# Kernel optimization log

Measured on AMD Instinct MI355X. Metric: run time of the kernel, lower is better.

The kernel has to match this reference:

```python
import jax, jax.numpy as jnp
import numpy as np

N_SRC0, N_FTRS, N_HID, N_CLS = 200000, 128, 1500, 64
E0, E1 = 1600000, 500000
RES0, RES1 = 50000, 10000


def sage_conv(x, src, tgt, res_size, W_root, W_neigh, b):
    # mean aggregation of neighbor (source) features onto the first res_size target nodes
    msg = x[src]                                              # [E, F] gather
    summed = jax.ops.segment_sum(msg, tgt, num_segments=res_size)   # [res, F]
    cnt = jax.ops.segment_sum(jnp.ones((src.shape[0],), x.dtype), tgt, num_segments=res_size)
    mean = summed / jnp.maximum(cnt, 1.0)[:, None]
    return x[:res_size] @ W_root + mean @ W_neigh + b


def setup_inputs() -> dict:
    key = jax.random.key(0)
    ks = jax.random.split(key, 12)
    x = jax.random.normal(ks[0], (N_SRC0, N_FTRS), dtype=jnp.float32)
    edge_src0 = jax.random.randint(ks[1], (E0,), 0, N_SRC0)
    edge_tgt0 = jax.random.randint(ks[2], (E0,), 0, RES0)
    edge_src1 = jax.random.randint(ks[3], (E1,), 0, RES0)
    edge_tgt1 = jax.random.randint(ks[4], (E1,), 0, RES1)
    s1 = 1.0 / np.sqrt(N_FTRS)
    s2 = 1.0 / np.sqrt(N_HID)
    W1_root = jax.random.uniform(ks[5], (N_FTRS, N_HID), jnp.float32, -s1, s1)
    W1_neigh = jax.random.uniform(ks[6], (N_FTRS, N_HID), jnp.float32, -s1, s1)
    b1 = jax.random.uniform(ks[7], (N_HID,), jnp.float32, -s1, s1)
    W2_root = jax.random.uniform(ks[8], (N_HID, N_CLS), jnp.float32, -s2, s2)
    W2_neigh = jax.random.uniform(ks[9], (N_HID, N_CLS), jnp.float32, -s2, s2)
    b2 = jax.random.uniform(ks[10], (N_CLS,), jnp.float32, -s2, s2)
    return {
        "x": x,
        "W1_root": W1_root, "W1_neigh": W1_neigh, "b1": b1,
        "W2_root": W2_root, "W2_neigh": W2_neigh, "b2": b2,
        "edge_src0": edge_src0, "edge_tgt0": edge_tgt0,
        "edge_src1": edge_src1, "edge_tgt1": edge_tgt1,
        "res0": RES0, "res1": RES1,
    }


def reference(x, W1_root, W1_neigh, b1, W2_root, W2_neigh, b2,
              edge_src0, edge_tgt0, edge_src1, edge_tgt1, res0, res1):
    h = sage_conv(x, edge_src0, edge_tgt0, res0, W1_root, W1_neigh, b1)  # [res0, H]
    h = jax.nn.relu(h)
    # dropout p=0.5 is identity in eval mode
    out = sage_conv(h, edge_src1, edge_tgt1, res1, W2_root, W2_neigh, b2)  # [res1, C]
    return jax.nn.log_softmax(out, axis=1)
```

## Files before the change

kernel.cpp:

```cpp
#include <hip/hip_runtime.h>
#include <hip/hip_bf16.h>
#include <cstdint>
#include <cstddef>

#define NSRC   200000
#define NF     128
#define NHID   1500
#define NHIDP  1536
#define NCLS   64
#define E0N    1600000
#define E1N    500000
#define RES0   50000
#define RES1   10000

#define CH     4096
#define NCH0   ((E0N + CH - 1) / CH)
#define NCH1   ((E1N + CH - 1) / CH)
#define NB0    ((RES0 + 255) / 256)
#define NB1    ((RES1 + 255) / 256)

#define PREP_BLOCKS  ((256 * NHIDP + 128 * NHIDP + NHIDP + 255) / 256)
#define COPYX_BLOCKS ((NSRC * NF) / (256 * 8))

typedef __bf16 bf16x8 __attribute__((ext_vector_type(8)));
typedef float  f32x4  __attribute__((ext_vector_type(4)));
typedef unsigned short u16x8 __attribute__((ext_vector_type(8)));
typedef unsigned int u32;
typedef unsigned long long u64;

__device__ __forceinline__ unsigned short f2bf(float f) {
    union { float f; unsigned u; } v; v.f = f;
    unsigned r = v.u + 0x7fffu + ((v.u >> 16) & 1u);
    return (unsigned short)(r >> 16);
}
__device__ __forceinline__ float bf2f(unsigned short b) {
    union { u32 u; float f; } v; v.u = ((u32)b) << 16;
    return v.f;
}

__device__ __forceinline__ void lds_dma16(const void* g, void* lds) {
    __builtin_amdgcn_global_load_lds(
        (const __attribute__((address_space(1))) unsigned int*)g,
        (__attribute__((address_space(3))) unsigned int*)lds, 16, 0, 0);
}

__device__ __forceinline__ void raw_barrier() {
    __asm__ volatile("s_barrier" ::: "memory");
}
__device__ __forceinline__ void wait_vm4() {
    __asm__ volatile("s_waitcnt vmcnt(4)" ::: "memory");
}
__device__ __forceinline__ void wait_vm0() {
    __asm__ volatile("s_waitcnt vmcnt(0)" ::: "memory");
}
__device__ __forceinline__ void wait_lgkm0() {
    __asm__ volatile("s_waitcnt lgkmcnt(0)" ::: "memory");
}

__global__ __launch_bounds__(256) void setup_kernel(
        const float* __restrict__ x, unsigned short* __restrict__ xbf,
        const float* __restrict__ W1r, const float* __restrict__ W1n,
        const float* __restrict__ b1,
        const float* __restrict__ W2r, const float* __restrict__ W2n,
        unsigned short* __restrict__ WcatT, unsigned short* __restrict__ W2catT,
        float* __restrict__ b1e) {
    int bid = blockIdx.x;
    if (bid < PREP_BLOCKS) {
        int id = bid * 256 + threadIdx.x;
        if (id < 256 * NHIDP) {
            int n = id >> 8, k = id & 255;
            float v = 0.f;
            if (n < NHID) v = (k < NF) ? W1r[k * NHID + n] : W1n[(k - NF) * NHID + n];
            WcatT[n * 256 + k] = f2bf(v);
        } else {
            int id2 = id - 256 * NHIDP;
            if (id2 < 128 * NHIDP) {
                int n = id2 / NHIDP, k = id2 % NHIDP;
                float v = 0.f;
                if (k < NHID) v = (n < 64) ? W2n[k * 64 + n] : W2r[k * 64 + (n - 64)];
                W2catT[n * NHIDP + k] = f2bf(v);
            } else {
                int c = id2 - 128 * NHIDP;
                if (c < NHIDP) b1e[c] = (c < NHID) ? b1[c] : 0.f;
            }
        }
    } else {
        size_t i = ((size_t)(bid - PREP_BLOCKS) * 256 + threadIdx.x) * 8;
        const float4* s = (const float4*)(x + i);
        float4 a = s[0], b = s[1];
        u16x8 o;
        o[0] = f2bf(a.x); o[1] = f2bf(a.y); o[2] = f2bf(a.z); o[3] = f2bf(a.w);
        o[4] = f2bf(b.x); o[5] = f2bf(b.y); o[6] = f2bf(b.z); o[7] = f2bf(b.w);
        *(u16x8*)(xbf + i) = o;
    }
}

__device__ __forceinline__ void p1a_body(const int* __restrict__ tgt, int n,
                                         int nb, u32* __restrict__ H, int c) {
    __shared__ u32 lhist[256];
    int tid = threadIdx.x;
    lhist[tid] = 0;
    __syncthreads();
#pragma unroll
    for (int it = 0; it < CH / 256; ++it) {
        int i = c * CH + it * 256 + tid;
        if (i < n) atomicAdd(&lhist[((u32)tgt[i]) >> 8], 1u);
    }
    __syncthreads();
    if (tid < nb) H[c * nb + tid] = lhist[tid];
}

__global__ __launch_bounds__(256) void p1a_both_kernel(
        const int* __restrict__ t0, const int* __restrict__ t1,
        u32* __restrict__ H1, u32* __restrict__ H2) {
    int b = blockIdx.x;
    if (b < NCH0) p1a_body(t0, E0N, NB0, H1, b);
    else          p1a_body(t1, E1N, NB1, H2, b - NCH0);
}

__device__ __forceinline__ void bscan_body(const u32* __restrict__ H,
                                           int nch, int nb, int b,
                                           u32* __restrict__ base_rel,
                                           u32* __restrict__ Bsum) {
    __shared__ u32 part[512];
    int t = threadIdx.x;
    part[t] = (t < nch) ? H[t * nb + b] : 0u;
    __syncthreads();
    for (int d = 1; d < 512; d <<= 1) {
        u32 v = part[t];
        u32 add = (t >= d) ? part[t - d] : 0u;
        __syncthreads();
        part[t] = v + add;
        __syncthreads();
    }
    if (t < nch) base_rel[t * nb + b] = (t == 0) ? 0u : part[t - 1];
    if (t == 0) Bsum[b] = part[nch - 1];
}

__global__ __launch_bounds__(512) void bscan_both_kernel(
        const u32* __restrict__ H1, u32* __restrict__ base1, u32* __restrict__ Bsum1,
        const u32* __restrict__ H2, u32* __restrict__ base2, u32* __restrict__ Bsum2) {
    int b = blockIdx.x;
    if (b < NB0) bscan_body(H1, NCH0, NB0, b, base1, Bsum1);
    else         bscan_body(H2, NCH1, NB1, b - NB0, base2, Bsum2);
}

__global__ __launch_bounds__(256) void boff_kernel(const u32* __restrict__ Bsum1,
                                                   u32* __restrict__ boff1, int nb1,
                                                   const u32* __restrict__ Bsum2,
                                                   u32* __restrict__ boff2, int nb2) {
    const u32* B = blockIdx.x ? Bsum2 : Bsum1;
    u32* O = blockIdx.x ? boff2 : boff1;
    int nb = blockIdx.x ? nb2 : nb1;
    __shared__ u32 part[256];
    int t = threadIdx.x;
    part[t] = (t < nb) ? B[t] : 0u;
    __syncthreads();
    for (int d = 1; d < 256; d <<= 1) {
        u32 v = part[t];
        u32 add = (t >= d) ? part[t - d] : 0u;
        __syncthreads();
        part[t] = v + add;
        __syncthreads();
    }
    if (t < nb) O[t] = (t == 0) ? 0u : part[t - 1];
}

__device__ __forceinline__ void p1b_body(const int* __restrict__ src,
                                         const int* __restrict__ tgt, int n,
                                         int nb, const u32* __restrict__ base_rel,
                                         const u32* __restrict__ boff,
                                         u64* __restrict__ bucketed, int c) {
    __shared__ u32 lcur[256];
    __shared__ u32 lbase[256];
    int tid = threadIdx.x;
    lcur[tid] = 0;
    if (tid < nb) lbase[tid] = base_rel[c * nb + tid] + boff[tid];
    __syncthreads();
#pragma unroll
    for (int it = 0; it < CH / 256; ++it) {
        int i = c * CH + it * 256 + tid;
        if (i < n) {
            u32 t = (u32)tgt[i];
            u32 s = (u32)src[i];
            u32 b = t >> 8;
            u32 r = atomicAdd(&lcur[b], 1u);
            bucketed[lbase[b] + r] = ((u64)t << 32) | (u64)s;
        }
    }
}

__global__ __launch_bounds__(256) void p1b_both_kernel(
        const int* __restrict__ s0, const int* __restrict__ t0,
        const u32* __restrict__ base1, const u32* __restrict__ boff1,
        u64* __restrict__ bkt1,
        const int* __restrict__ s1, const int* __restrict__ t1,
        const u32* __restrict__ base2, const u32* __restrict__ boff2,
        u64* __restrict__ bkt2) {
    int b = blockIdx.x;
    if (b < NCH0) p1b_body(s0, t0, E0N, NB0, base1, boff1, bkt1, b);
    else          p1b_body(s1, t1, E1N, NB1, base2, boff2, bkt2, b - NCH0);
}

__device__ __forceinline__ void p2_body(const u64* __restrict__ bucketed,
                                        const u32* __restrict__ boff,
                                        int nb, int res, int etot,
                                        int* __restrict__ csr,
                                        u32* __restrict__ off_out,
                                        u32* __restrict__ cnt_out, int b) {
    __shared__ u32 lhist[256];
    __shared__ u32 part[256];
    __shared__ u32 cur[256];
    int tid = threadIdx.x;
    u32 start = boff[b];
    u32 end = (b == nb - 1) ? (u32)etot : boff[b + 1];
    u32 count = end - start;
    if (tid < 256) lhist[tid] = 0;
    __syncthreads();
    for (u32 i = tid; i < count; i += 1024) {
        u32 t = (u32)(bucketed[start + i] >> 32);
        atomicAdd(&lhist[t & 255u], 1u);
    }
    __syncthreads();
    if (tid < 256) part[tid] = lhist[tid];
    __syncthreads();
    for (int d = 1; d < 256; d <<= 1) {
        u32 v = (tid < 256) ? part[tid] : 0u;
        u32 add = (tid >= d && tid < 256) ? part[tid - d] : 0u;
        __syncthreads();
        if (tid < 256) part[tid] = v + add;
        __syncthreads();
    }
    if (tid < 256) {
        u32 excl = (tid == 0) ? 0u : part[tid - 1];
        cur[tid] = excl;
        int tg = (b << 8) + tid;
        if (tg < res) {
            off_out[tg] = start + excl;
            cnt_out[tg] = lhist[tid];
        }
    }
    __syncthreads();
    for (u32 i = tid; i < count; i += 1024) {
        u64 pr = bucketed[start + i];
        u32 lt = ((u32)(pr >> 32)) & 255u;
        u32 r = atomicAdd(&cur[lt], 1u);
        csr[start + r] = (int)(u32)pr;
    }
}

__global__ __launch_bounds__(1024) void p2_both_kernel(
        const u64* __restrict__ bkt1, const u32* __restrict__ boff1,
        int* __restrict__ csr1, u32* __restrict__ off1, u32* __restrict__ cnt1,
        const u64* __restrict__ bkt2, const u32* __restrict__ boff2,
        int* __restrict__ csr2, u32* __restrict__ off2, u32* __restrict__ cnt2) {
    int b = blockIdx.x;
    if (b < NB0) p2_body(bkt1, boff1, NB0, RES0, E0N, csr1, off1, cnt1, b);
    else         p2_body(bkt2, boff2, NB1, RES1, E1N, csr2, off2, cnt2, b - NB0);
}

__global__ __launch_bounds__(256) void agg1_csr_kernel(
        const unsigned short* __restrict__ xbf, const int* __restrict__ csr,
        const u32* __restrict__ off, const u32* __restrict__ cnt,
        unsigned short* __restrict__ mean1) {
    int row = blockIdx.x * 4 + (threadIdx.x >> 6);
    int lane = threadIdx.x & 63;
    if (row >= RES0) return;
    int q = lane >> 4, c16 = lane & 15;
    u32 base = off[row], deg = cnt[row];
    float acc[8] = {};
    u32 e = 0;
    for (; e + 8 <= deg; e += 8) {
        int s0 = csr[base + e + q];
        int s1 = csr[base + e + 4 + q];
        u16x8 v0 = *(const u16x8*)(xbf + (size_t)s0 * NF + c16 * 8);
        u16x8 v1 = *(const u16x8*)(xbf + (size_t)s1 * NF + c16 * 8);
#pragma unroll
        for (int i = 0; i < 8; ++i) acc[i] += bf2f(v0[i]) + bf2f(v1[i]);
    }
    for (; e + 4 <= deg; e += 4) {
        int s0 = csr[base + e + q];
        u16x8 v0 = *(const u16x8*)(xbf + (size_t)s0 * NF + c16 * 8);
#pragma unroll
        for (int i = 0; i < 8; ++i) acc[i] += bf2f(v0[i]);
    }
    if (e < deg) {
        bool valid = (e + q) < deg;
        int s0 = csr[base + (valid ? e + q : e)];
        u16x8 v0 = *(const u16x8*)(xbf + (size_t)s0 * NF + c16 * 8);
        if (valid) {
#pragma unroll
            for (int i = 0; i < 8; ++i) acc[i] += bf2f(v0[i]);
        }
    }
#pragma unroll
    for (int i = 0; i < 8; ++i) {
        acc[i] += __shfl_xor(acc[i], 32, 64);
        acc[i] += __shfl_xor(acc[i], 16, 64);
    }
    if (q == 0) {
        float inv = 1.0f / fmaxf((float)deg, 1.0f);
        u16x8 o;
#pragma unroll
        for (int i = 0; i < 8; ++i) o[i] = f2bf(acc[i] * inv);
        *(u16x8*)(mean1 + (size_t)row * NF + c16 * 8) = o;
    }
}

__device__ __forceinline__ void stage_chunk(
        const unsigned short* __restrict__ xbf, const unsigned short* __restrict__ mean1,
        const unsigned short* __restrict__ WcatT, int m0, int j, int kt,
        unsigned short* As, unsigned short* Bs, int wid, int lane) {
    int ksel = kt * 32;
    const unsigned short* srcA = (ksel < 128)
        ? xbf + (size_t)m0 * NF + ksel
        : mean1 + (size_t)m0 * NF + (ksel - 128);
#pragma unroll
    for (int ci = 0; ci < 2; ++ci) {
        int cb = ci * 256 + wid * 64;
        int chunk = cb + lane;
        int n = chunk >> 2, kc = chunk & 3;
        lds_dma16(srcA + (size_t)n * NF + kc * 8, &As[cb * 8]);
    }
    const unsigned short* srcB = WcatT + (size_t)(j * 128) * 256 + ksel;
#pragma unroll
    for (int ci = 0; ci < 2; ++ci) {
        int cb = ci * 256 + wid * 64;
        int chunk = cb + lane;
        int n = chunk >> 2, kc = chunk & 3;
        lds_dma16(srcB + (size_t)n * 256 + kc * 8, &Bs[cb * 8]);
    }
}

__global__ __launch_bounds__(256, 2) void fused_gemm_kernel(
        const unsigned short* __restrict__ xbf, const unsigned short* __restrict__ mean1,
        const unsigned short* __restrict__ WcatT, const float* __restrict__ b1e,
        const unsigned short* __restrict__ W2catT,
        unsigned short* __restrict__ pnbf, float* __restrict__ root64) {
    __shared__ __align__(16) unsigned short As[3][128 * 32];
    __shared__ __align__(16) unsigned short Bs[3][128 * 32];
    __shared__ __align__(16) unsigned short Ht[128 * 128];

    int m0 = blockIdx.x * 128;
    int tid = threadIdx.x;
    int lane = tid & 63, wid = tid >> 6;
    int wm = wid >> 1, wn = wid & 1;
    int quad = lane >> 4, l15 = lane & 15;

    f32x4 pacc[4][4] = {};

    stage_chunk(xbf, mean1, WcatT, m0, 0, 0, As[0], Bs[0], wid, lane);
    stage_chunk(xbf, mean1, WcatT, m0, 0, 1, As[1], Bs[1], wid, lane);

#pragma unroll 1
    for (int jj = 0; jj < 12; ++jj) {
        const int j = jj;
        f32x4 hacc[4][4] = {};
#pragma unroll
        for (int kt = 0; kt < 8; ++kt) {
            const int g = jj * 8 + kt;
            if (g == 95) wait_vm0(); else wait_vm4();
            raw_barrier();
            if (g + 2 < 96) {
                int g2 = g + 2;
                stage_chunk(xbf, mean1, WcatT, m0, g2 >> 3, g2 & 7,
                            As[g2 % 3], Bs[g2 % 3], wid, lane);
            }
            const unsigned short* Asb = As[g % 3];
            const unsigned short* Bsb = Bs[g % 3];
            bf16x8 a[4], b[4];
#pragma unroll
            for (int mi = 0; mi < 4; ++mi)
                a[mi] = *(const bf16x8*)(&Asb[(wm * 64 + mi * 16 + l15) * 32 + quad * 8]);
#pragma unroll
            for (int ni = 0; ni < 4; ++ni)
                b[ni] = *(const bf16x8*)(&Bsb[(wn * 64 + ni * 16 + l15) * 32 + quad * 8]);
#pragma unroll
            for (int mi = 0; mi < 4; ++mi)
#pragma unroll
                for (int ni = 0; ni < 4; ++ni)
                    hacc[mi][ni] = __builtin_amdgcn_mfma_f32_16x16x32_bf16(b[ni], a[mi], hacc[mi][ni], 0, 0, 0);
        }
#pragma unroll
        for (int ni = 0; ni < 4; ++ni) {
            int n0 = wn * 64 + ni * 16 + quad * 4;
            float4 bv = *(const float4*)(b1e + j * 128 + n0);
#pragma unroll
            for (int mi = 0; mi < 4; ++mi) {
                int m = wm * 64 + mi * 16 + l15;
                int gsw = ((n0 >> 3) ^ (m & 15));
                ushort4 o;
                o.x = f2bf(fmaxf(hacc[mi][ni][0] + bv.x, 0.f));
                o.y = f2bf(fmaxf(hacc[mi][ni][1] + bv.y, 0.f));
                o.z = f2bf(fmaxf(hacc[mi][ni][2] + bv.z, 0.f));
                o.w = f2bf(fmaxf(hacc[mi][ni][3] + bv.w, 0.f));
                *(ushort4*)(&Ht[m * 128 + gsw * 8 + (n0 & 7)]) = o;
            }
        }
        wait_lgkm0();
        raw_barrier();
#pragma unroll
        for (int kk2 = 0; kk2 < 128; kk2 += 32) {
            bf16x8 a2[4], b2[4];
#pragma unroll
            for (int mi = 0; mi < 4; ++mi) {
                int m = wm * 64 + mi * 16 + l15;
                int gr = (kk2 >> 3) + quad;
                int gsw = gr ^ (m & 15);
                a2[mi] = *(const bf16x8*)(&Ht[m * 128 + gsw * 8]);
            }
#pragma unroll
            for (int ni = 0; ni < 4; ++ni)
                b2[ni] = *(const bf16x8*)(W2catT + (size_t)(wn * 64 + ni * 16 + l15) * NHIDP
                                          + j * 128 + kk2 + quad * 8);
#pragma unroll
            for (int mi = 0; mi < 4; ++mi)
#pragma unroll
                for (int ni = 0; ni < 4; ++ni)
                    pacc[mi][ni] = __builtin_amdgcn_mfma_f32_16x16x32_bf16(b2[ni], a2[mi], pacc[mi][ni], 0, 0, 0);
        }
    }

#pragma unroll
    for (int mi = 0; mi < 4; ++mi) {
        int gr = m0 + wm * 64 + mi * 16 + l15;
        if (gr < RES0) {
#pragma unroll
            for (int ni = 0; ni < 4; ++ni) {
                f32x4 s = pacc[mi][ni];
                int c0 = ni * 16 + quad * 4;
                if (wn == 0) {
                    uint2 o;
                    o.x = (u32)f2bf(s[0]) | ((u32)f2bf(s[1]) << 16);
                    o.y = (u32)f2bf(s[2]) | ((u32)f2bf(s[3]) << 16);
                    *(uint2*)(pnbf + (size_t)gr * 64 + c0) = o;
                } else if (gr < RES1) {
                    *(f32x4*)(root64 + (size_t)gr * 64 + c0) = s;
                }
            }
        }
    }
}

__global__ __launch_bounds__(256) void final_csr_kernel(
        const unsigned short* __restrict__ pnbf, const float* __restrict__ root64,
        const int* __restrict__ csr, const u32* __restrict__ off,
        const u32* __restrict__ cnt, const float* __restrict__ b2,
        float* __restrict__ out) {
    int row = blockIdx.x * 4 + (threadIdx.x >> 6);
    int lane = threadIdx.x & 63;
    if (row >= RES1) return;
    int es = lane >> 3, c8 = lane & 7;
    u32 base = off[row], deg = cnt[row];
    float acc[8] = {};
    u32 e = 0;
    for (; e + 8 <= deg; e += 8) {
        int s = csr[base + e + es];
        u16x8 v = *(const u16x8*)(pnbf + (size_t)s * 64 + c8 * 8);
#pragma unroll
        for (int i = 0; i < 8; ++i) acc[i] += bf2f(v[i]);
    }
    if (e < deg) {
        bool valid = (e + es) < deg;
        int s = csr[base + (valid ? e + es : e)];
        u16x8 v = *(const u16x8*)(pnbf + (size_t)s * 64 + c8 * 8);
        if (valid) {
#pragma unroll
            for (int i = 0; i < 8; ++i) acc[i] += bf2f(v[i]);
        }
    }
#pragma unroll
    for (int i = 0; i < 8; ++i) {
        acc[i] += __shfl_xor(acc[i], 32, 64);
        acc[i] += __shfl_xor(acc[i], 16, 64);
        acc[i] += __shfl_xor(acc[i], 8, 64);
    }
    float inv = 1.0f / fmaxf((float)deg, 1.0f);
    float v[8];
    const float* rp = root64 + (size_t)row * 64 + c8 * 8;
#pragma unroll
    for (int i = 0; i < 8; ++i) v[i] = rp[i] + acc[i] * inv + b2[c8 * 8 + i];
    float m = v[0];
#pragma unroll
    for (int i = 1; i < 8; ++i) m = fmaxf(m, v[i]);
    m = fmaxf(m, __shfl_xor(m, 1, 64));
    m = fmaxf(m, __shfl_xor(m, 2, 64));
    m = fmaxf(m, __shfl_xor(m, 4, 64));
    float s = 0.f;
#pragma unroll
    for (int i = 0; i < 8; ++i) s += expf(v[i] - m);
    s += __shfl_xor(s, 1, 64);
    s += __shfl_xor(s, 2, 64);
    s += __shfl_xor(s, 4, 64);
    if (es == 0) {
        float lg = logf(s);
        f32x4 o0, o1;
#pragma unroll
        for (int i = 0; i < 4; ++i) { o0[i] = v[i] - m - lg; o1[i] = v[i + 4] - m - lg; }
        *(f32x4*)(&out[(size_t)row * 64 + c8 * 8])     = o0;
        *(f32x4*)(&out[(size_t)row * 64 + c8 * 8 + 4]) = o1;
    }
}

extern "C" void kernel_launch(void* const* d_in, const int* in_sizes, int n_in,
                              void* d_out, int out_size, void* d_ws, size_t ws_size,
                              hipStream_t stream) {
    const float* x   = (const float*)d_in[0];
    const float* W1r = (const float*)d_in[1];
    const float* W1n = (const float*)d_in[2];
    const float* b1  = (const float*)d_in[3];
    const float* W2r = (const float*)d_in[4];
    const float* W2n = (const float*)d_in[5];
    const float* b2  = (const float*)d_in[6];
    const int* es0 = (const int*)d_in[7];
    const int* et0 = (const int*)d_in[8];
    const int* es1 = (const int*)d_in[9];
    const int* et1 = (const int*)d_in[10];
    float* out = (float*)d_out;

    char* ws = (char*)d_ws;
    size_t off_ = 0;
    auto alloc = [&](size_t bytes) {
        void* ptr = ws + off_;
        off_ = (off_ + bytes + 255) & ~(size_t)255;
        return ptr;
    };
    u64* bkt1  = (u64*)alloc((size_t)E0N * 8);
    u64* bkt2  = (u64*)alloc((size_t)E1N * 8);
    int* csr1  = (int*)alloc((size_t)E0N * 4);
    u32* H1    = (u32*)alloc((size_t)NCH0 * NB0 * 4);
    u32* base1 = (u32*)alloc((size_t)NCH0 * NB0 * 4);
    u32* H2    = (u32*)alloc((size_t)NCH1 * NB1 * 4);
    u32* base2 = (u32*)alloc((size_t)NCH1 * NB1 * 4);
    u32* Bsum1 = (u32*)alloc((size_t)NB0 * 4);
    u32* Bsum2 = (u32*)alloc((size_t)NB1 * 4);
    u32* boff1 = (u32*)alloc((size_t)NB0 * 4);
    u32* boff2 = (u32*)alloc((size_t)NB1 * 4);
    u32* off1  = (u32*)alloc((size_t)RES0 * 4);
    u32* cnt1  = (u32*)alloc((size_t)RES0 * 4);
    int* csr2  = (int*)alloc((size_t)E1N * 4);
    u32* off2  = (u32*)alloc((size_t)RES1 * 4);
    u32* cnt2  = (u32*)alloc((size_t)RES1 * 4);
    unsigned short* xbf    = (unsigned short*)alloc((size_t)NSRC * NF * 2);
    unsigned short* mean1  = (unsigned short*)alloc((size_t)(RES0 + 128) * NF * 2);
    unsigned short* WcatT  = (unsigned short*)alloc((size_t)NHIDP * 256 * 2);
    unsigned short* W2catT = (unsigned short*)alloc((size_t)128 * NHIDP * 2);
    float*          b1e    = (float*)alloc((size_t)NHIDP * 4);
    unsigned short* pnbf   = (unsigned short*)alloc((size_t)RES0 * 64 * 2);
    float*          root64 = (float*)alloc((size_t)RES1 * 64 * 4);

    setup_kernel<<<PREP_BLOCKS + COPYX_BLOCKS, 256, 0, stream>>>(
        x, xbf, W1r, W1n, b1, W2r, W2n, WcatT, W2catT, b1e);

    p1a_both_kernel<<<NCH0 + NCH1, 256, 0, stream>>>(et0, et1, H1, H2);
    bscan_both_kernel<<<NB0 + NB1, 512, 0, stream>>>(H1, base1, Bsum1, H2, base2, Bsum2);
    boff_kernel<<<2, 256, 0, stream>>>(Bsum1, boff1, NB0, Bsum2, boff2, NB1);
    p1b_both_kernel<<<NCH0 + NCH1, 256, 0, stream>>>(
        es0, et0, base1, boff1, bkt1, es1, et1, base2, boff2, bkt2);
    p2_both_kernel<<<NB0 + NB1, 1024, 0, stream>>>(
        bkt1, boff1, csr1, off1, cnt1, bkt2, boff2, csr2, off2, cnt2);

    agg1_csr_kernel<<<(RES0 + 3) / 4, 256, 0, stream>>>(
        xbf, csr1, off1, cnt1, mean1);

    fused_gemm_kernel<<<(RES0 + 127) / 128, 256, 0, stream>>>(
        xbf, mean1, WcatT, b1e, W2catT, pnbf, root64);

    final_csr_kernel<<<(RES1 + 3) / 4, 256, 0, stream>>>(
        pnbf, root64, csr2, off2, cnt2, b2, out);
}
```

Measured before the change: 435.5 us.

## Keep hidden tile in registers, feeding second GEMM directly from MFMA accumulators

The fused GEMM now gives each wave 32 full rows of the 128-wide hidden tile instead of a 64x64 quadrant. The bias+ReLU result can then be packed to bf16 in registers with v_cvt_pk_bf16 and used directly as the A operand of the second GEMM, with no LDS staging of H. This drops the 32KB Ht buffer and its barrier. W2 is pre-permuted in setup to match the accumulator-derived k ordering, the A/B LDS tiles get an XOR swizzle to cut bank conflicts, and s_setprio is raised around the MFMA blocks. The cost is that every wave now reads all 128 B columns from LDS, and W2 is loaded from global memory per wave.

New measurement: 438.5 us. About the same (+0.7%).

```diff
diff --git a/kernel.cpp b/kernel.cpp
--- a/kernel.cpp
+++ b/kernel.cpp
@@ -38,6 +38,12 @@
     return v.f;
 }
 
+__device__ __forceinline__ u32 cvt_pk_bf16(float lo, float hi) {
+    u32 r;
+    asm("v_cvt_pk_bf16_f32 %0, %1, %2" : "=v"(r) : "v"(lo), "v"(hi));
+    return r;
+}
+
 __device__ __forceinline__ void lds_dma16(const void* g, void* lds) {
     __builtin_amdgcn_global_load_lds(
         (const __attribute__((address_space(1))) unsigned int*)g,
@@ -52,9 +58,6 @@
 }
 __device__ __forceinline__ void wait_vm0() {
     __asm__ volatile("s_waitcnt vmcnt(0)" ::: "memory");
-}
-__device__ __forceinline__ void wait_lgkm0() {
-    __asm__ volatile("s_waitcnt lgkmcnt(0)" ::: "memory");
 }
 
 __global__ __launch_bounds__(256) void setup_kernel(
@@ -62,7 +65,7 @@
         const float* __restrict__ W1r, const float* __restrict__ W1n,
         const float* __restrict__ b1,
         const float* __restrict__ W2r, const float* __restrict__ W2n,
-        unsigned short* __restrict__ WcatT, unsigned short* __restrict__ W2catT,
+        unsigned short* __restrict__ WcatT, unsigned short* __restrict__ W2f,
         float* __restrict__ b1e) {
     int bid = blockIdx.x;
     if (bid < PREP_BLOCKS) {
@@ -78,7 +81,10 @@
                 int n = id2 / NHIDP, k = id2 % NHIDP;
                 float v = 0.f;
                 if (k < NHID) v = (n < 64) ? W2n[k * 64 + n] : W2r[k * 64 + (n - 64)];
-                W2catT[n * NHIDP + k] = f2bf(v);
+                int j = k >> 7, w = k & 127;
+                int kk = w >> 5, r = w & 31;
+                int hi = r >> 4, qd = (r >> 2) & 3, e = r & 3;
+                W2f[(((size_t)(j * 4 + kk) * 128 + n) * 32) + qd * 8 + hi * 4 + e] = f2bf(v);
             } else {
                 int c = id2 - 128 * NHIDP;
                 if (c < NHIDP) b1e[c] = (c < NHID) ? b1[c] : 0.f;
@@ -319,7 +325,7 @@
     for (int ci = 0; ci < 2; ++ci) {
         int cb = ci * 256 + wid * 64;
         int chunk = cb + lane;
-        int n = chunk >> 2, kc = chunk & 3;
+        int n = chunk >> 2, kc = (chunk & 3) ^ (n & 3);
         lds_dma16(srcA + (size_t)n * NF + kc * 8, &As[cb * 8]);
     }
     const unsigned short* srcB = WcatT + (size_t)(j * 128) * 256 + ksel;
@@ -327,7 +333,7 @@
     for (int ci = 0; ci < 2; ++ci) {
         int cb = ci * 256 + wid * 64;
         int chunk = cb + lane;
-        int n = chunk >> 2, kc = chunk & 3;
+        int n = chunk >> 2, kc = (chunk & 3) ^ (n & 3);
         lds_dma16(srcB + (size_t)n * 256 + kc * 8, &Bs[cb * 8]);
     }
 }
@@ -335,19 +341,19 @@
 __global__ __launch_bounds__(256, 2) void fused_gemm_kernel(
         const unsigned short* __restrict__ xbf, const unsigned short* __restrict__ mean1,
         const unsigned short* __restrict__ WcatT, const float* __restrict__ b1e,
-        const unsigned short* __restrict__ W2catT,
+        const unsigned short* __restrict__ W2f,
         unsigned short* __restrict__ pnbf, float* __restrict__ root64) {
     __shared__ __align__(16) unsigned short As[3][128 * 32];
     __shared__ __align__(16) unsigned short Bs[3][128 * 32];
-    __shared__ __align__(16) unsigned short Ht[128 * 128];
 
     int m0 = blockIdx.x * 128;
     int tid = threadIdx.x;
     int lane = tid & 63, wid = tid >> 6;
-    int wm = wid >> 1, wn = wid & 1;
+    int wm = wid;
     int quad = lane >> 4, l15 = lane & 15;
-
-    f32x4 pacc[4][4] = {};
+    const int csw = (quad ^ (l15 & 3)) * 8;
+
+    f32x4 pacc[2][8] = {};
 
     stage_chunk(xbf, mean1, WcatT, m0, 0, 0, As[0], Bs[0], wid, lane);
     stage_chunk(xbf, mean1, WcatT, m0, 0, 1, As[1], Bs[1], wid, lane);
@@ -355,7 +361,7 @@
 #pragma unroll 1
     for (int jj = 0; jj < 12; ++jj) {
         const int j = jj;
-        f32x4 hacc[4][4] = {};
+        f32x4 hacc[2][8] = {};
 #pragma unroll
         for (int kt = 0; kt < 8; ++kt) {
             const int g = jj * 8 + kt;
@@ -368,74 +374,74 @@
             }
             const unsigned short* Asb = As[g % 3];
             const unsigned short* Bsb = Bs[g % 3];
-            bf16x8 a[4], b[4];
-#pragma unroll
-            for (int mi = 0; mi < 4; ++mi)
-                a[mi] = *(const bf16x8*)(&Asb[(wm * 64 + mi * 16 + l15) * 32 + quad * 8]);
-#pragma unroll
-            for (int ni = 0; ni < 4; ++ni)
-                b[ni] = *(const bf16x8*)(&Bsb[(wn * 64 + ni * 16 + l15) * 32 + quad * 8]);
-#pragma unroll
-            for (int mi = 0; mi < 4; ++mi)
-#pragma unroll
-                for (int ni = 0; ni < 4; ++ni)
+            bf16x8 a[2], b[8];
+#pragma unroll
+            for (int mi = 0; mi < 2; ++mi)
+                a[mi] = *(const bf16x8*)(&Asb[(wm * 32 + mi * 16 + l15) * 32 + csw]);
+#pragma unroll
+            for (int ni = 0; ni < 8; ++ni)
+                b[ni] = *(const bf16x8*)(&Bsb[(ni * 16 + l15) * 32 + csw]);
+            __builtin_amdgcn_s_setprio(1);
+#pragma unroll
+            for (int mi = 0; mi < 2; ++mi)
+#pragma unroll
+                for (int ni = 0; ni < 8; ++ni)
                     hacc[mi][ni] = __builtin_amdgcn_mfma_f32_16x16x32_bf16(b[ni], a[mi], hacc[mi][ni], 0, 0, 0);
-        }
-#pragma unroll
-        for (int ni = 0; ni < 4; ++ni) {
-            int n0 = wn * 64 + ni * 16 + quad * 4;
-            float4 bv = *(const float4*)(b1e + j * 128 + n0);
-#pragma unroll
-            for (int mi = 0; mi < 4; ++mi) {
-                int m = wm * 64 + mi * 16 + l15;
-                int gsw = ((n0 >> 3) ^ (m & 15));
-                ushort4 o;
-                o.x = f2bf(fmaxf(hacc[mi][ni][0] + bv.x, 0.f));
-                o.y = f2bf(fmaxf(hacc[mi][ni][1] + bv.y, 0.f));
-                o.z = f2bf(fmaxf(hacc[mi][ni][2] + bv.z, 0.f));
-                o.w = f2bf(fmaxf(hacc[mi][ni][3] + bv.w, 0.f));
-                *(ushort4*)(&Ht[m * 128 + gsw * 8 + (n0 & 7)]) = o;
+            __builtin_amdgcn_s_setprio(0);
+        }
+
+        u32 a2w[2][4][4];
+#pragma unroll
+        for (int ni = 0; ni < 8; ++ni) {
+            float4 bv = *(const float4*)(b1e + j * 128 + ni * 16 + quad * 4);
+#pragma unroll
+            for (int mi = 0; mi < 2; ++mi) {
+                f32x4 h = hacc[mi][ni];
+                float h0 = fmaxf(h[0] + bv.x, 0.f);
+                float h1 = fmaxf(h[1] + bv.y, 0.f);
+                float h2 = fmaxf(h[2] + bv.z, 0.f);
+                float h3 = fmaxf(h[3] + bv.w, 0.f);
+                a2w[mi][ni >> 1][(ni & 1) * 2 + 0] = cvt_pk_bf16(h0, h1);
+                a2w[mi][ni >> 1][(ni & 1) * 2 + 1] = cvt_pk_bf16(h2, h3);
             }
         }
-        wait_lgkm0();
-        raw_barrier();
-#pragma unroll
-        for (int kk2 = 0; kk2 < 128; kk2 += 32) {
-            bf16x8 a2[4], b2[4];
-#pragma unroll
-            for (int mi = 0; mi < 4; ++mi) {
-                int m = wm * 64 + mi * 16 + l15;
-                int gr = (kk2 >> 3) + quad;
-                int gsw = gr ^ (m & 15);
-                a2[mi] = *(const bf16x8*)(&Ht[m * 128 + gsw * 8]);
+        __builtin_amdgcn_s_setprio(1);
+#pragma unroll
+        for (int kk = 0; kk < 4; ++kk) {
+            union U { u32 w[4]; bf16x8 v; uint4 q; };
+            U A2[2];
+#pragma unroll
+            for (int mi = 0; mi < 2; ++mi)
+#pragma unroll
+                for (int w = 0; w < 4; ++w) A2[mi].w[w] = a2w[mi][kk][w];
+            const unsigned short* wp =
+                W2f + ((size_t)(j * 4 + kk) * 128) * 32 + (size_t)quad * 8;
+#pragma unroll
+            for (int ni2 = 0; ni2 < 8; ++ni2) {
+                U B2;
+                B2.q = *(const uint4*)(wp + (size_t)(ni2 * 16 + l15) * 32);
+#pragma unroll
+                for (int mi = 0; mi < 2; ++mi)
+                    pacc[mi][ni2] = __builtin_amdgcn_mfma_f32_16x16x32_bf16(B2.v, A2[mi].v, pacc[mi][ni2], 0, 0, 0);
             }
-#pragma unroll
-            for (int ni = 0; ni < 4; ++ni)
-                b2[ni] = *(const bf16x8*)(W2catT + (size_t)(wn * 64 + ni * 16 + l15) * NHIDP
-                                          + j * 128 + kk2 + quad * 8);
-#pragma unroll
-            for (int mi = 0; mi < 4; ++mi)
-#pragma unroll
-                for (int ni = 0; ni < 4; ++ni)
-                    pacc[mi][ni] = __builtin_amdgcn_mfma_f32_16x16x32_bf16(b2[ni], a2[mi], pacc[mi][ni], 0, 0, 0);
-        }
-    }
-
-#pragma unroll
-    for (int mi = 0; mi < 4; ++mi) {
-        int gr = m0 + wm * 64 + mi * 16 + l15;
+        }
+        __builtin_amdgcn_s_setprio(0);
+    }
+
+#pragma unroll
+    for (int mi = 0; mi < 2; ++mi) {
+        int gr = m0 + wm * 32 + mi * 16 + l15;
         if (gr < RES0) {
 #pragma unroll
-            for (int ni = 0; ni < 4; ++ni) {
-                f32x4 s = pacc[mi][ni];
-                int c0 = ni * 16 + quad * 4;
-                if (wn == 0) {
+            for (int ni2 = 0; ni2 < 8; ++ni2) {
+                f32x4 s = pacc[mi][ni2];
+                if (ni2 < 4) {
                     uint2 o;
                     o.x = (u32)f2bf(s[0]) | ((u32)f2bf(s[1]) << 16);
                     o.y = (u32)f2bf(s[2]) | ((u32)f2bf(s[3]) << 16);
-                    *(uint2*)(pnbf + (size_t)gr * 64 + c0) = o;
+                    *(uint2*)(pnbf + (size_t)gr * 64 + ni2 * 16 + quad * 4) = o;
                 } else if (gr < RES1) {
-                    *(f32x4*)(root64 + (size_t)gr * 64 + c0) = s;
+                    *(f32x4*)(root64 + (size_t)gr * 64 + (ni2 - 4) * 16 + quad * 4) = s;
                 }
             }
         }
@@ -544,13 +550,13 @@
     unsigned short* xbf    = (unsigned short*)alloc((size_t)NSRC * NF * 2);
     unsigned short* mean1  = (unsigned short*)alloc((size_t)(RES0 + 128) * NF * 2);
     unsigned short* WcatT  = (unsigned short*)alloc((size_t)NHIDP * 256 * 2);
-    unsigned short* W2catT = (unsigned short*)alloc((size_t)128 * NHIDP * 2);
+    unsigned short* W2f    = (unsigned short*)alloc((size_t)128 * NHIDP * 2);
     float*          b1e    = (float*)alloc((size_t)NHIDP * 4);
     unsigned short* pnbf   = (unsigned short*)alloc((size_t)RES0 * 64 * 2);
     float*          root64 = (float*)alloc((size_t)RES1 * 64 * 4);
 
     setup_kernel<<<PREP_BLOCKS + COPYX_BLOCKS, 256, 0, stream>>>(
-        x, xbf, W1r, W1n, b1, W2r, W2n, WcatT, W2catT, b1e);
+        x, xbf, W1r, W1n, b1, W2r, W2n, WcatT, W2f, b1e);
 
     p1a_both_kernel<<<NCH0 + NCH1, 256, 0, stream>>>(et0, et1, H1, H2);
     bscan_both_kernel<<<NB0 + NB1, 512, 0, stream>>>(H1, base1, Bsum1, H2, base2, Bsum2);
@@ -564,7 +570,7 @@
         xbf, csr1, off1, cnt1, mean1);
 
     fused_gemm_kernel<<<(RES0 + 127) / 128, 256, 0, stream>>>(
-        xbf, mean1, WcatT, b1e, W2catT, pnbf, root64);
+        xbf, mean1, WcatT, b1e, W2f, pnbf, root64);
 
     final_csr_kernel<<<(RES1 + 3) / 4, 256, 0, stream>>>(
         pnbf, root64, csr2, off2, cnt2, b2, out);
```
